# Optimization experiments

Hardware: AMD Instinct MI355X
Metric: run time of the kernel (lower is better)

Reference implementation:

```python
import jax, jax.numpy as jnp
import numpy as np

N_IN, N_H, N_OUT = 256, 2048, 256
BATCH, T = 64, 512


def setup_inputs() -> dict:
    key = jax.random.key(0)
    k_u, k_uh, k_hh, k_hy, k_h0 = jax.random.split(key, 5)
    u = jax.random.normal(k_u, (BATCH, T, N_IN), dtype=jnp.float32)
    # sparse_normal_weights with p=1: N(0, g^2/N_src), returned transposed -> (N_src, N_dst)
    W_uh = jax.random.normal(k_uh, (N_IN, N_H), dtype=jnp.float32) / np.sqrt(N_IN)
    W_hh = jax.random.normal(k_hh, (N_H, N_H), dtype=jnp.float32) / np.sqrt(N_H)
    W_hy = jax.random.normal(k_hy, (N_H, N_OUT), dtype=jnp.float32) / np.sqrt(N_H)
    b_h = jnp.zeros((N_H,), dtype=jnp.float32)
    b_y = jnp.zeros((N_OUT,), dtype=jnp.float32)
    # h0 ~ Uniform[-1, 1] (tanh branch)
    h0 = jax.random.uniform(k_h0, (N_H,), dtype=jnp.float32, minval=-1.0, maxval=1.0)
    tau = jnp.ones((N_H,), dtype=jnp.float32)
    return {"u": u, "W_uh": W_uh, "W_hh": W_hh, "W_hy": W_hy,
            "b_h": b_h, "b_y": b_y, "h0": h0, "tau": tau}


def reference(u, W_uh, W_hh, W_hy, b_h, b_y, h0, tau):
    # Leaky CTRNN, f_h=tanh, f_out=softmax, noise=0.0, h0=None path
    alpha = 1.0 / tau                      # (N_h,)
    h0c = jnp.clip(h0, -1.0, 1.0)          # clip_initial_state for tanh
    batch = u.shape[0]
    h_init = jnp.broadcast_to(h0c, (batch, N_H))

    def step(h, u_t):
        pre = h @ W_hh + u_t @ W_uh + b_h          # (B, N_h)
        h_new = (1.0 - alpha) * h + alpha * jnp.tanh(pre)
        y_t = jax.nn.softmax(h_new @ W_hy + b_y, axis=1)  # (B, N_out)
        return h_new, y_t

    u_t_first = jnp.swapaxes(u, 0, 1)              # (T, B, N_in)
    _, y = jax.lax.scan(step, h_init, u_t_first)   # y: (T, B, N_out)
    return jnp.swapaxes(y, 0, 1)                   # (B, T, N_out)
```

## Files before the change

kernel.cpp:

```cpp
#include <hip/hip_runtime.h>
#include <hip/hip_fp16.h>

#define N_INP 256
#define NH    2048
#define NOUT  256
#define BB    64
#define TT    512
#define GRIDN 128
#define CNT_STRIDE 16

typedef __bf16 bf16x8 __attribute__((ext_vector_type(8)));
typedef float  f32x4  __attribute__((ext_vector_type(4)));

__device__ __forceinline__ unsigned short f2bf(float f) {
  unsigned u = __float_as_uint(f);
  u += 0x7fffu + ((u >> 16) & 1u);
  return (unsigned short)(u >> 16);
}

__device__ __forceinline__ float fast_tanh(float x) {
  x = fminf(9.0f, fmaxf(-9.0f, x));
  float e = __expf(2.0f * x);
  return (e - 1.0f) / (e + 1.0f);
}

__device__ __forceinline__ f32x4 mfma16(uint4 a, uint4 b, f32x4 c) {
  return __builtin_amdgcn_mfma_f32_16x16x32_bf16(
      __builtin_bit_cast(bf16x8, a), __builtin_bit_cast(bf16x8, b), c, 0, 0, 0);
}

__device__ __forceinline__ void gbar(unsigned* cnt, int idx) {
  __builtin_amdgcn_s_waitcnt(0);
  __syncthreads();
  if (threadIdx.x == 0) {
    unsigned* c = cnt + (size_t)idx * CNT_STRIDE;
    __hip_atomic_fetch_add(c, 1u, __ATOMIC_RELAXED, __HIP_MEMORY_SCOPE_AGENT);
    while (__hip_atomic_load(c, __ATOMIC_RELAXED, __HIP_MEMORY_SCOPE_AGENT) < GRIDN)
      __builtin_amdgcn_s_sleep(1);
  }
  __syncthreads();
}

__global__ void k_zero(unsigned* __restrict__ cnt, int n) {
  int i = blockIdx.x * 256 + threadIdx.x;
  if (i < n) cnt[i] = 0;
}

__global__ void k_ut(const float* __restrict__ u, unsigned short* __restrict__ ut) {
  int idx = blockIdx.x * 256 + threadIdx.x;
  int k4 = idx & 63;
  int rowbt = idx >> 6;
  int t = rowbt >> 6, b = rowbt & 63;
  float4 f = *(const float4*)(u + ((size_t)b * TT + t) * N_INP + k4 * 4);
  uint2 pk;
  pk.x = f2bf(f.x) | ((unsigned)f2bf(f.y) << 16);
  pk.y = f2bf(f.z) | ((unsigned)f2bf(f.w) << 16);
  *(uint2*)(ut + (size_t)rowbt * N_INP + k4 * 4) = pk;
}

__global__ void k_swz(const float* __restrict__ W, unsigned short* __restrict__ Wf, int N) {
  int lane = threadIdx.x;
  int nt16 = N >> 4;
  int kb = blockIdx.x / nt16;
  int nt = blockIdx.x - kb * nt16;
  int k0 = kb * 32 + ((lane >> 4) << 3);
  int c  = nt * 16 + (lane & 15);
  unsigned short v[8];
#pragma unroll
  for (int j = 0; j < 8; ++j) v[j] = f2bf(W[(size_t)(k0 + j) * N + c]);
  uint4 p;
  p.x = v[0] | ((unsigned)v[1] << 16);
  p.y = v[2] | ((unsigned)v[3] << 16);
  p.z = v[4] | ((unsigned)v[5] << 16);
  p.w = v[6] | ((unsigned)v[7] << 16);
  ((uint4*)Wf)[(size_t)blockIdx.x * 64 + lane] = p;
}

__global__ __launch_bounds__(256) void k_step(
    const float* __restrict__ Whh, const float* __restrict__ Wuh,
    const float* __restrict__ b_h, const float* __restrict__ tau,
    const float* __restrict__ h0, const unsigned short* __restrict__ ut,
    unsigned short* __restrict__ H, unsigned* __restrict__ cnt) {
  __shared__ unsigned short lds[64 * 64 * 8];
  const int cgp = blockIdx.x;
  const int tid = threadIdx.x;
  const int wave = tid >> 6;
  const int lane = tid & 63;
  const int q = lane >> 4, p = lane & 15;

  for (int s = tid; s < 64 * 64; s += 256) {
    int kb = s >> 6, l = s & 63;
    int k0 = kb * 32 + ((l >> 4) << 3);
    int c = cgp * 16 + (l & 15);
    unsigned short v[8];
#pragma unroll
    for (int j = 0; j < 8; ++j) v[j] = f2bf(Whh[(size_t)(k0 + j) * NH + c]);
    uint4 pk;
    pk.x = v[0] | ((unsigned)v[1] << 16);
    pk.y = v[2] | ((unsigned)v[3] << 16);
    pk.z = v[4] | ((unsigned)v[5] << 16);
    pk.w = v[6] | ((unsigned)v[7] << 16);
    ((uint4*)lds)[s] = pk;
  }

  const int c = cgp * 16 + p;
  const float al = 1.0f / tau[c];
  const float onem = 1.0f - al;
  const float bh_c = b_h[c];
  const float h0c = fminf(1.0f, fmaxf(-1.0f, h0[c]));
  float hprev[4] = {h0c, h0c, h0c, h0c};
  const int rbase = wave * 16;
  const bool even = (p & 1) == 0;
  const int halfc = cgp * 8 + (p >> 1);
  unsigned* H32 = (unsigned*)H;

  uint4 wu[8];
#pragma unroll
  for (int kb = 0; kb < 8; ++kb) {
    unsigned short v[8];
#pragma unroll
    for (int j = 0; j < 8; ++j)
      v[j] = f2bf(Wuh[(size_t)(kb * 32 + q * 8 + j) * NH + c]);
    wu[kb].x = v[0] | ((unsigned)v[1] << 16);
    wu[kb].y = v[2] | ((unsigned)v[3] << 16);
    wu[kb].z = v[4] | ((unsigned)v[5] << 16);
    wu[kb].w = v[6] | ((unsigned)v[7] << 16);
  }

  {
    unsigned mine = f2bf(h0c);
    unsigned other = (unsigned)__shfl_xor((int)mine, 1);
    unsigned pk0 = even ? (mine | (other << 16)) : (other | (mine << 16));
    if (even) {
#pragma unroll
      for (int r = 0; r < 4; ++r)
        __hip_atomic_store(H32 + (size_t)(rbase + q * 4 + r) * (NH / 2) + halfc,
                           pk0, __ATOMIC_RELAXED, __HIP_MEMORY_SCOPE_AGENT);
    }
  }

  gbar(cnt, 0);

  const uint4* ldsv = (const uint4*)lds;
  for (int t = 0; t < TT; ++t) {
    f32x4 acc[4];
#pragma unroll
    for (int j = 0; j < 4; ++j) acc[j] = (f32x4){0.f, 0.f, 0.f, 0.f};

    const uint4* Au = (const uint4*)(ut + ((size_t)t * BB + rbase + p) * N_INP + q * 8);
#pragma unroll
    for (int kb = 0; kb < 8; ++kb)
      acc[kb & 3] = mfma16(Au[kb * 4], wu[kb], acc[kb & 3]);

    const uint4* Ar = (const uint4*)(H + (size_t)t * BB * NH + (size_t)(rbase + p) * NH + q * 8);
    uint4 a[8];
#pragma unroll
    for (int j = 0; j < 8; ++j) a[j] = Ar[j * 4];
#pragma unroll
    for (int kb = 0; kb < 64; kb += 8) {
      uint4 an[8];
      if (kb < 56) {
#pragma unroll
        for (int j = 0; j < 8; ++j) an[j] = Ar[(kb + 8 + j) * 4];
      }
#pragma unroll
      for (int j = 0; j < 8; ++j)
        acc[j & 3] = mfma16(a[j], ldsv[(kb + j) * 64 + lane], acc[j & 3]);
      if (kb < 56) {
#pragma unroll
        for (int j = 0; j < 8; ++j) a[j] = an[j];
      }
    }

    unsigned* H32n = H32 + (size_t)(t + 1) * BB * (NH / 2);
#pragma unroll
    for (int r = 0; r < 4; ++r) {
      float pre = acc[0][r] + acc[1][r] + acc[2][r] + acc[3][r] + bh_c;
      float hn = onem * hprev[r] + al * fast_tanh(pre);
      hprev[r] = hn;
      unsigned mine = f2bf(hn);
      unsigned other = (unsigned)__shfl_xor((int)mine, 1);
      unsigned pk = even ? (mine | (other << 16)) : (other | (mine << 16));
      if (even)
        __hip_atomic_store(H32n + (size_t)(rbase + q * 4 + r) * (NH / 2) + halfc,
                           pk, __ATOMIC_RELAXED, __HIP_MEMORY_SCOPE_AGENT);
    }
    gbar(cnt, t + 1);
  }
}

__global__ __launch_bounds__(256) void k_y(
    const unsigned short* __restrict__ H, const unsigned short* __restrict__ Wyf,
    const float* __restrict__ b_y, float* __restrict__ out) {
  int wave = threadIdx.x >> 6, lane = threadIdx.x & 63;
  int q = lane >> 4, p = lane & 15;
  int R = blockIdx.x * 64 + wave * 16;
  const uint4* A = (const uint4*)(H + (size_t)(R + BB + p) * NH + q * 8);
  const uint4* Bf = (const uint4*)Wyf;
  f32x4 acc[16];
#pragma unroll
  for (int nt = 0; nt < 16; ++nt) acc[nt] = (f32x4){0.f, 0.f, 0.f, 0.f};
  for (int kb = 0; kb < 64; ++kb) {
    uint4 a = A[kb * 4];
#pragma unroll
    for (int nt = 0; nt < 16; ++nt) {
      uint4 b = Bf[(size_t)(kb * 16 + nt) * 64 + lane];
      acc[nt] = mfma16(a, b, acc[nt]);
    }
  }
  float bb[16];
#pragma unroll
  for (int nt = 0; nt < 16; ++nt) bb[nt] = b_y[nt * 16 + p];
#pragma unroll
  for (int r = 0; r < 4; ++r) {
    int row = R + q * 4 + r;
    int tI = row >> 6, bI = row & 63;
    float lg[16];
    float mx = -1e30f;
#pragma unroll
    for (int nt = 0; nt < 16; ++nt) { lg[nt] = acc[nt][r] + bb[nt]; mx = fmaxf(mx, lg[nt]); }
#pragma unroll
    for (int d = 1; d < 16; d <<= 1) mx = fmaxf(mx, __shfl_xor(mx, d));
    float s = 0.f;
#pragma unroll
    for (int nt = 0; nt < 16; ++nt) { lg[nt] = __expf(lg[nt] - mx); s += lg[nt]; }
#pragma unroll
    for (int d = 1; d < 16; d <<= 1) s += __shfl_xor(s, d);
    float inv = 1.0f / s;
    float* orow = out + ((size_t)bI * TT + tI) * NOUT;
#pragma unroll
    for (int nt = 0; nt < 16; ++nt) orow[nt * 16 + p] = lg[nt] * inv;
  }
}

extern "C" void kernel_launch(void* const* d_in, const int* in_sizes, int n_in,
                              void* d_out, int out_size, void* d_ws, size_t ws_size,
                              hipStream_t stream) {
  (void)in_sizes; (void)n_in; (void)out_size; (void)ws_size;
  const float* u   = (const float*)d_in[0];
  const float* Wuh = (const float*)d_in[1];
  const float* Whh = (const float*)d_in[2];
  const float* Why = (const float*)d_in[3];
  const float* b_h = (const float*)d_in[4];
  const float* b_y = (const float*)d_in[5];
  const float* h0  = (const float*)d_in[6];
  const float* tau = (const float*)d_in[7];
  float* out = (float*)d_out;

  char* ws = (char*)d_ws;
  unsigned short* H = (unsigned short*)ws;
  size_t off = (size_t)(TT + 1) * BB * NH * 2;
  unsigned short* ut = (unsigned short*)(ws + off);
  off += (size_t)TT * BB * N_INP * 2;
  unsigned short* Wyf = (unsigned short*)(ws + off);
  off += (size_t)NH * NOUT * 2;
  unsigned* cnt = (unsigned*)(ws + off);

  const int ncnt = (TT + 1) * CNT_STRIDE;
  k_zero<<<dim3((ncnt + 255) / 256), dim3(256), 0, stream>>>(cnt, ncnt);
  k_ut<<<dim3(8192), dim3(256), 0, stream>>>(u, ut);
  k_swz<<<dim3((NH / 32) * (NOUT / 16)), dim3(64), 0, stream>>>(Why, Wyf, NOUT);

  void* args[] = {(void*)&Whh, (void*)&Wuh, (void*)&b_h, (void*)&tau,
                  (void*)&h0, (void*)&ut, (void*)&H, (void*)&cnt};
  hipLaunchCooperativeKernel((const void*)k_step, dim3(GRIDN), dim3(256), args, 0, stream);

  k_y<<<dim3(512), dim3(256), 0, stream>>>(H, Wyf, b_y, out);
}
```

Measured before the change: 6.009 ms.

## Replace atomic-counter grid barrier with split flag/release barrier and overlap input GEMM

The single contended atomic counter per step is replaced by per-block arrival flags that block 0 polls with one wave. Block 0 then publishes release flags, spread over 8 cache lines, that the other blocks spin on. The barrier is split into an arrive phase and a wait phase, and the next step's u_t·W_uh MFMA work runs between them, hiding part of the barrier latency. This adds a two-hop master-coordinated barrier and more workspace zeroing. Its correctness relies on relaxed atomics plus waitcnt for visibility of H.

New measurement: 5.287 ms. 12.0% less time.

```diff
diff --git a/kernel.cpp b/kernel.cpp
--- a/kernel.cpp
+++ b/kernel.cpp
@@ -7,7 +7,7 @@
 #define BB    64
 #define TT    512
 #define GRIDN 128
-#define CNT_STRIDE 16
+#define REL_STRIDE 32
 
 typedef __bf16 bf16x8 __attribute__((ext_vector_type(8)));
 typedef float  f32x4  __attribute__((ext_vector_type(4)));
@@ -29,21 +29,46 @@
       __builtin_bit_cast(bf16x8, a), __builtin_bit_cast(bf16x8, b), c, 0, 0, 0);
 }
 
-__device__ __forceinline__ void gbar(unsigned* cnt, int idx) {
+__device__ __forceinline__ void bar_arrive(unsigned* __restrict__ flags, int s) {
   __builtin_amdgcn_s_waitcnt(0);
   __syncthreads();
-  if (threadIdx.x == 0) {
-    unsigned* c = cnt + (size_t)idx * CNT_STRIDE;
-    __hip_atomic_fetch_add(c, 1u, __ATOMIC_RELAXED, __HIP_MEMORY_SCOPE_AGENT);
-    while (__hip_atomic_load(c, __ATOMIC_RELAXED, __HIP_MEMORY_SCOPE_AGENT) < GRIDN)
-      __builtin_amdgcn_s_sleep(1);
-  }
-  __syncthreads();
-}
-
-__global__ void k_zero(unsigned* __restrict__ cnt, int n) {
+  if (blockIdx.x != 0 && threadIdx.x == 0)
+    __hip_atomic_store(flags + (size_t)s * GRIDN + blockIdx.x, 1u,
+                       __ATOMIC_RELAXED, __HIP_MEMORY_SCOPE_AGENT);
+}
+
+__device__ __forceinline__ void bar_wait(unsigned* __restrict__ flags,
+                                         unsigned* __restrict__ rel, int s) {
+  if (blockIdx.x == 0) {
+    int tid = threadIdx.x;
+    if (tid < 64) {
+      const unsigned* f = flags + (size_t)s * GRIDN;
+      for (;;) {
+        unsigned a = (tid == 0) ? 1u
+            : __hip_atomic_load(f + tid, __ATOMIC_RELAXED, __HIP_MEMORY_SCOPE_AGENT);
+        unsigned b = __hip_atomic_load(f + 64 + tid, __ATOMIC_RELAXED,
+                                       __HIP_MEMORY_SCOPE_AGENT);
+        if (__all(a != 0 && b != 0)) break;
+        __builtin_amdgcn_s_sleep(1);
+      }
+      if (tid < 8)
+        __hip_atomic_store(rel + ((size_t)s * 8 + tid) * REL_STRIDE, 1u,
+                           __ATOMIC_RELAXED, __HIP_MEMORY_SCOPE_AGENT);
+    }
+    __syncthreads();
+  } else {
+    if (threadIdx.x == 0) {
+      unsigned* r = rel + ((size_t)s * 8 + (blockIdx.x & 7)) * REL_STRIDE;
+      while (!__hip_atomic_load(r, __ATOMIC_RELAXED, __HIP_MEMORY_SCOPE_AGENT))
+        __builtin_amdgcn_s_sleep(1);
+    }
+    __syncthreads();
+  }
+}
+
+__global__ void k_zero(unsigned* __restrict__ p, int n) {
   int i = blockIdx.x * 256 + threadIdx.x;
-  if (i < n) cnt[i] = 0;
+  if (i < n) p[i] = 0;
 }
 
 __global__ void k_ut(const float* __restrict__ u, unsigned short* __restrict__ ut) {
@@ -80,7 +105,8 @@
     const float* __restrict__ Whh, const float* __restrict__ Wuh,
     const float* __restrict__ b_h, const float* __restrict__ tau,
     const float* __restrict__ h0, const unsigned short* __restrict__ ut,
-    unsigned short* __restrict__ H, unsigned* __restrict__ cnt) {
+    unsigned short* __restrict__ H, unsigned* __restrict__ flags,
+    unsigned* __restrict__ rel) {
   __shared__ unsigned short lds[64 * 64 * 8];
   const int cgp = blockIdx.x;
   const int tid = threadIdx.x;
@@ -139,19 +165,21 @@
     }
   }
 
-  gbar(cnt, 0);
-
   const uint4* ldsv = (const uint4*)lds;
-  for (int t = 0; t < TT; ++t) {
-    f32x4 acc[4];
+  f32x4 acc[4];
+
+  bar_arrive(flags, 0);
+  {
+    const uint4* Au = (const uint4*)(ut + ((size_t)(rbase + p)) * N_INP + q * 8);
 #pragma unroll
     for (int j = 0; j < 4; ++j) acc[j] = (f32x4){0.f, 0.f, 0.f, 0.f};
-
-    const uint4* Au = (const uint4*)(ut + ((size_t)t * BB + rbase + p) * N_INP + q * 8);
 #pragma unroll
     for (int kb = 0; kb < 8; ++kb)
       acc[kb & 3] = mfma16(Au[kb * 4], wu[kb], acc[kb & 3]);
-
+  }
+  bar_wait(flags, rel, 0);
+
+  for (int t = 0; t < TT; ++t) {
     const uint4* Ar = (const uint4*)(H + (size_t)t * BB * NH + (size_t)(rbase + p) * NH + q * 8);
     uint4 a[8];
 #pragma unroll
@@ -185,7 +213,17 @@
         __hip_atomic_store(H32n + (size_t)(rbase + q * 4 + r) * (NH / 2) + halfc,
                            pk, __ATOMIC_RELAXED, __HIP_MEMORY_SCOPE_AGENT);
     }
-    gbar(cnt, t + 1);
+
+    if (t + 1 < TT) {
+      bar_arrive(flags, t + 1);
+      const uint4* Au = (const uint4*)(ut + ((size_t)(t + 1) * BB + rbase + p) * N_INP + q * 8);
+#pragma unroll
+      for (int j = 0; j < 4; ++j) acc[j] = (f32x4){0.f, 0.f, 0.f, 0.f};
+#pragma unroll
+      for (int kb = 0; kb < 8; ++kb)
+        acc[kb & 3] = mfma16(Au[kb * 4], wu[kb], acc[kb & 3]);
+      bar_wait(flags, rel, t + 1);
+    }
   }
 }
 
@@ -254,15 +292,17 @@
   off += (size_t)TT * BB * N_INP * 2;
   unsigned short* Wyf = (unsigned short*)(ws + off);
   off += (size_t)NH * NOUT * 2;
-  unsigned* cnt = (unsigned*)(ws + off);
-
-  const int ncnt = (TT + 1) * CNT_STRIDE;
-  k_zero<<<dim3((ncnt + 255) / 256), dim3(256), 0, stream>>>(cnt, ncnt);
+  unsigned* flags = (unsigned*)(ws + off);
+  off += (size_t)(TT + 1) * GRIDN * 4;
+  unsigned* rel = (unsigned*)(ws + off);
+
+  const int nz = (TT + 1) * GRIDN + (TT + 1) * 8 * REL_STRIDE;
+  k_zero<<<dim3((nz + 255) / 256), dim3(256), 0, stream>>>(flags, nz);
   k_ut<<<dim3(8192), dim3(256), 0, stream>>>(u, ut);
   k_swz<<<dim3((NH / 32) * (NOUT / 16)), dim3(64), 0, stream>>>(Why, Wyf, NOUT);
 
   void* args[] = {(void*)&Whh, (void*)&Wuh, (void*)&b_h, (void*)&tau,
-                  (void*)&h0, (void*)&ut, (void*)&H, (void*)&cnt};
+                  (void*)&h0, (void*)&ut, (void*)&H, (void*)&flags, (void*)&rel};
   hipLaunchCooperativeKernel((const void*)k_step, dim3(GRIDN), dim3(256), args, 0, stream);
 
   k_y<<<dim3(512), dim3(256), 0, stream>>>(H, Wyf, b_y, out);
```
